# Kernel optimization log

Hardware: AMD Instinct MI355X
Metric: run time of the kernel (lower is better)

## Reference

```python
import jax, jax.numpy as jnp
import numpy as np

# ---- module hyperparameters (from init_kwargs) ----
K_CURV = 1.0      # Lorentz curvature k
MAX_NORM = 1000.0 # rescale_to_max cap on space-norm (assumed)
KSIZE = 5
STRIDE = 2
PAD = 2
IN_CH = 257       # includes time dim -> 256 space channels
OUT_CH = 257
LIN_FEATS = (IN_CH - 1) * KSIZE + 1  # 1281
EPS = 1e-8


def _add_time(space):
    # time = sqrt(k + ||space||^2), concat on last axis
    time = jnp.sqrt(K_CURV + jnp.sum(space * space, axis=-1, keepdims=True))
    return jnp.concatenate([time, space], axis=-1)


def _rescale_to_max(x):
    # clamp space-norm to MAX_NORM, then recompute valid time component
    space = x[..., 1:]
    norm = jnp.sqrt(jnp.sum(space * space, axis=-1, keepdims=True))
    scale = jnp.minimum(1.0, MAX_NORM / jnp.maximum(norm, EPS))
    return _add_time(space * scale)


def setup_inputs() -> dict:
    key = jax.random.key(0)
    kx, kw, kb = jax.random.split(key, 3)
    x = jax.random.normal(kx, (16, 8192, IN_CH), dtype=jnp.float32)
    W = jax.random.normal(kw, (OUT_CH, LIN_FEATS), dtype=jnp.float32) * 0.02
    b = jax.random.normal(kb, (OUT_CH,), dtype=jnp.float32) * 0.01
    return {"x": x, "W": W, "b": b}


def reference(x, W, b):
    B, L, C = x.shape
    # pad length dim with zeros (time channel of padded frames is clamped in
    # torch, but the time channel is discarded before add_time, so only the
    # space channels matter)
    xp = jnp.pad(x, ((0, 0), (PAD, PAD), (0, 0)))
    space = xp[..., 1:]                                  # (B, Lp, C-1)
    Lp = L + 2 * PAD
    n_frames = (Lp - KSIZE) // STRIDE + 1
    # im2col gather: (n_frames, K) window indices
    idx = jnp.arange(n_frames)[:, None] * STRIDE + jnp.arange(KSIZE)[None, :]
    patches = space[:, idx, :]                           # (B, n, K, C-1)
    # torch reorders to kernel-major (k, c) layout before add_time
    ps = patches.reshape(B, n_frames, KSIZE * (C - 1))   # (B, n, K*(C-1))
    pk = _add_time(ps)                                   # (B, n, lin_feats)
    out = jnp.einsum('bnf,of->bno', pk, W) + b           # LorentzProjection
    out = _add_time(out[..., 1:])                        # manifold.projx
    out = _rescale_to_max(out)                           # rescale_after=True
    return out
```

## Files before the change

### kernel.cpp

```cpp
#include <hip/hip_runtime.h>
#include <hip/hip_bf16.h>
#include <cstdint>
#include <cstddef>

namespace {

constexpr int BATCH = 16;
constexpr int LEN   = 8192;
constexpr int CIN   = 257;
constexpr int CS    = 256;
constexpr int NF    = 4096;
constexpr int LPAD  = LEN + 4;
constexpr int KG    = 1280;
constexpr int MT    = 64;

constexpr size_t XS_ELEMS  = (size_t)BATCH * LPAD * CS;
constexpr size_t XS_BYTES  = XS_ELEMS * 2;
constexpr size_t RSQ_OFF   = XS_BYTES;
constexpr size_t RSQ_BYTES = (size_t)BATCH * LPAD * 4;
constexpr size_t WT_OFF    = RSQ_OFF + RSQ_BYTES;
constexpr size_t WT_BYTES  = (size_t)CS * KG * 2;
constexpr size_t W0_OFF    = WT_OFF + WT_BYTES;
constexpr size_t WS_NEED   = W0_OFF + (size_t)CS * 4;

typedef __attribute__((ext_vector_type(8))) short short8;
typedef __attribute__((ext_vector_type(4))) float f32x4;

__device__ __forceinline__ unsigned short f2bf_bits(float f) {
  union { __hip_bfloat16 h; unsigned short u; } cv;
  cv.h = __float2bfloat16(f);
  return cv.u;
}

__device__ __forceinline__ void async_cp16(const void* g, void* l) {
  __builtin_amdgcn_global_load_lds(
      (const __attribute__((address_space(1))) void*)g,
      (__attribute__((address_space(3))) void*)l,
      16, 0, 0);
}

}

__global__ void prep_w_kernel(const float* __restrict__ W,
                              __hip_bfloat16* __restrict__ wt,
                              float* __restrict__ w0) {
  int n = blockIdx.x;
  const float* wrow = W + (size_t)(n + 1) * 1281;
  for (int k = threadIdx.x; k < KG; k += blockDim.x)
    wt[(size_t)n * KG + k] = __float2bfloat16(wrow[1 + k]);
  if (threadIdx.x == 0) w0[n] = wrow[0];
}

__global__ void prep_x_kernel(const float* __restrict__ x,
                              __hip_bfloat16* __restrict__ xs,
                              float* __restrict__ rowsq) {
  const int tid = threadIdx.x;
  const int bx  = blockIdx.x;
  if (bx < (BATCH * LEN) / 4) {
    int r    = bx * 4 + (tid >> 6);
    int lane = tid & 63;
    int b    = r >> 13;
    int t    = r & (LEN - 1);
    size_t tpg = (size_t)b * LPAD + 2 + t;
    const float* src = x + (size_t)r * CIN + 1 + lane * 4;
    float f0 = src[0], f1 = src[1], f2 = src[2], f3 = src[3];
    float s = f0 * f0 + f1 * f1 + f2 * f2 + f3 * f3;
    ushort4 pk;
    pk.x = f2bf_bits(f0); pk.y = f2bf_bits(f1);
    pk.z = f2bf_bits(f2); pk.w = f2bf_bits(f3);
    *(ushort4*)(xs + tpg * CS + lane * 4) = pk;
    for (int off = 32; off > 0; off >>= 1) s += __shfl_down(s, off);
    if (lane == 0) rowsq[tpg] = s;
  } else {
    for (int i = tid; i < 64 * 128; i += 256) {
      int row = i >> 7, u = i & 127;
      int b = row >> 2, j = row & 3;
      size_t tpg = (size_t)b * LPAD + (j < 2 ? j : 8192 + j);
      ((uint32_t*)xs)[tpg * 128 + u] = 0;
      if (u == 0) rowsq[tpg] = 0.0f;
    }
  }
}

__global__ __launch_bounds__(256, 3) void lorentz_gemm_kernel(
    const __hip_bfloat16* __restrict__ xs,
    const __hip_bfloat16* __restrict__ wt,
    const float* __restrict__ rowsq,
    const float* __restrict__ w0,
    const float* __restrict__ bvec,
    float* __restrict__ out) {
  __shared__ alignas(16) char lds[8192 + 32768];
  __shared__ alignas(16) float time0_s[64];
  __shared__ alignas(16) float normsq_s[64];
  char* A_lds = lds;
  char* B_lds = lds + 8192;

  const int tid   = threadIdx.x;
  const int w     = tid >> 6;
  const int lane  = tid & 63;
  const int row16 = lane & 15;
  const int q     = lane >> 4;

  const int bx    = blockIdx.x;
  const int b     = bx >> 6;
  const int Mbase = (bx & 63) * MT;

  const __hip_bfloat16* xsb = xs + ((size_t)b * LPAD + 2 * Mbase) * CS;

  f32x4 acc[4][4];
#pragma unroll
  for (int i = 0; i < 4; ++i)
#pragma unroll
    for (int j = 0; j < 4; ++j) acc[i][j] = (f32x4){0.f, 0.f, 0.f, 0.f};

  const int csw = (lane & 7) ^ (lane >> 3);

  for (int it = 0; it < 20; ++it) {
    const int kk = it >> 2;
    const int c0 = (it & 3) << 6;
    const int k0 = it << 6;
    __syncthreads();
#pragma unroll
    for (int j = 0; j < 2; ++j) {
      int m = w * 16 + j * 8 + (lane >> 3);
      const void* g = xsb + (size_t)(2 * m + kk) * CS + c0 + csw * 8;
      async_cp16(g, A_lds + (w * 2 + j) * 1024);
    }
#pragma unroll
    for (int j = 0; j < 8; ++j) {
      int n = w * 64 + j * 8 + (lane >> 3);
      const void* g = wt + (size_t)n * KG + k0 + csw * 8;
      async_cp16(g, B_lds + (w * 8 + j) * 1024);
    }
    __syncthreads();
#pragma unroll
    for (int s = 0; s < 2; ++s) {
      const int p = (s * 4 + q) ^ (lane & 7);
      short8 af[4], bf[4];
#pragma unroll
      for (int mt = 0; mt < 4; ++mt)
        af[mt] = *(const short8*)(A_lds + ((mt * 16 + row16) * 8 + p) * 16);
#pragma unroll
      for (int nt = 0; nt < 4; ++nt)
        bf[nt] = *(const short8*)(B_lds + ((w * 64 + nt * 16 + row16) * 8 + p) * 16);
#pragma unroll
      for (int mt = 0; mt < 4; ++mt)
#pragma unroll
        for (int nt = 0; nt < 4; ++nt)
          acc[mt][nt] = __builtin_amdgcn_mfma_f32_16x16x32_bf16(
              af[mt], bf[nt], acc[mt][nt], 0, 0, 0);
    }
  }

  if (tid < 64) {
    const float* rs = rowsq + (size_t)b * LPAD + 2 * (Mbase + tid);
    float s5 = rs[0] + rs[1] + rs[2] + rs[3] + rs[4];
    time0_s[tid] = sqrtf(1.0f + s5);
    normsq_s[tid] = 0.0f;
  }
  __syncthreads();

  float w0v[4], bv[4];
#pragma unroll
  for (int nt = 0; nt < 4; ++nt) {
    int n = w * 64 + nt * 16 + row16;
    w0v[nt] = w0[n];
    bv[nt]  = bvec[1 + n];
  }

#pragma unroll
  for (int mt = 0; mt < 4; ++mt) {
    f32x4 t4 = *(const f32x4*)&time0_s[mt * 16 + q * 4];
#pragma unroll
    for (int nt = 0; nt < 4; ++nt)
#pragma unroll
      for (int r = 0; r < 4; ++r)
        acc[mt][nt][r] = acc[mt][nt][r] + t4[r] * w0v[nt] + bv[nt];
#pragma unroll
    for (int r = 0; r < 4; ++r) {
      float ps = 0.f;
#pragma unroll
      for (int nt = 0; nt < 4; ++nt) ps += acc[mt][nt][r] * acc[mt][nt][r];
      ps += __shfl_xor(ps, 1);
      ps += __shfl_xor(ps, 2);
      ps += __shfl_xor(ps, 4);
      ps += __shfl_xor(ps, 8);
      if (row16 == 0) atomicAdd(&normsq_s[mt * 16 + q * 4 + r], ps);
    }
  }
  __syncthreads();

#pragma unroll
  for (int mt = 0; mt < 4; ++mt) {
#pragma unroll
    for (int r = 0; r < 4; ++r) {
      int m = mt * 16 + q * 4 + r;
      float nsq  = normsq_s[m];
      float norm = sqrtf(nsq);
      float scale = fminf(1.0f, 1000.0f / fmaxf(norm, 1e-8f));
      size_t ob = ((size_t)b * NF + Mbase + m) * 257;
#pragma unroll
      for (int nt = 0; nt < 4; ++nt) {
        int n = w * 64 + nt * 16 + row16;
        out[ob + 1 + n] = acc[mt][nt][r] * scale;
      }
    }
  }
  if (tid < 64) {
    float nsq  = normsq_s[tid];
    float norm = sqrtf(nsq);
    float scale = fminf(1.0f, 1000.0f / fmaxf(norm, 1e-8f));
    size_t ob = ((size_t)b * NF + Mbase + tid) * 257;
    out[ob] = sqrtf(1.0f + scale * scale * nsq);
  }
}

__global__ void fallback_kernel(const float* __restrict__ x,
                                const float* __restrict__ W,
                                const float* __restrict__ bvec,
                                float* __restrict__ out) {
  int fid = blockIdx.x;
  int b = fid >> 12;
  int g = fid & (NF - 1);
  __shared__ float patch[1280];
  __shared__ float red[256];
  int tid = threadIdx.x;
  float ss = 0.f;
  for (int k = tid; k < 1280; k += 256) {
    int kk = k >> 8, c = k & 255;
    int t = 2 * g + kk - 2;
    float v = (t >= 0 && t < LEN) ? x[((size_t)b * LEN + t) * CIN + 1 + c] : 0.f;
    patch[k] = v;
    ss += v * v;
  }
  red[tid] = ss;
  __syncthreads();
  for (int off = 128; off > 0; off >>= 1) {
    if (tid < off) red[tid] += red[tid + off];
    __syncthreads();
  }
  float time0 = sqrtf(1.f + red[0]);
  __syncthreads();
  const float* wrow = W + (size_t)(tid + 1) * 1281;
  float acc = time0 * wrow[0] + bvec[tid + 1];
  for (int k = 0; k < 1280; ++k) acc += wrow[1 + k] * patch[k];
  red[tid] = acc * acc;
  __syncthreads();
  for (int off = 128; off > 0; off >>= 1) {
    if (tid < off) red[tid] += red[tid + off];
    __syncthreads();
  }
  float nsq = red[0];
  float norm = sqrtf(nsq);
  float scale = fminf(1.f, 1000.f / fmaxf(norm, 1e-8f));
  size_t ob = ((size_t)b * NF + g) * 257;
  out[ob + 1 + tid] = acc * scale;
  if (tid == 0) out[ob] = sqrtf(1.f + scale * scale * nsq);
}

extern "C" void kernel_launch(void* const* d_in, const int* in_sizes, int n_in,
                              void* d_out, int out_size, void* d_ws, size_t ws_size,
                              hipStream_t stream) {
  const float* x  = (const float*)d_in[0];
  const float* W  = (const float*)d_in[1];
  const float* bv = (const float*)d_in[2];
  float* out = (float*)d_out;

  if (ws_size >= WS_NEED) {
    char* ws = (char*)d_ws;
    __hip_bfloat16* xs = (__hip_bfloat16*)ws;
    float* rowsq       = (float*)(ws + RSQ_OFF);
    __hip_bfloat16* wt = (__hip_bfloat16*)(ws + WT_OFF);
    float* w0          = (float*)(ws + W0_OFF);
    prep_w_kernel<<<256, 256, 0, stream>>>(W, wt, w0);
    prep_x_kernel<<<(BATCH * LEN) / 4 + 1, 256, 0, stream>>>(x, xs, rowsq);
    lorentz_gemm_kernel<<<BATCH * (NF / MT), 256, 0, stream>>>(xs, wt, rowsq, w0, bv, out);
  } else {
    fallback_kernel<<<BATCH * NF, 256, 0, stream>>>(x, W, bv, out);
  }
}
```

Before: 281.1 us.

## Double GEMM M-tile to 128 with 8 waves and stage prep_x rows through LDS

The GEMM kernel now covers 128 output frames per block with 512 threads arranged as 2×4 waves. Each W tile loaded into LDS is therefore reused across twice as many rows, which halves the per-frame W traffic and block count. Separately, prep_x now loads 16 full input rows per block into shared memory with coalesced float4 reads, then converts them to bf16 with 16-byte stores. This replaces the earlier misaligned scalar loads. The larger block uses more LDS and registers per block, and the launch-bounds change could reduce occupancy.

Measured after the change: 272.3 us. 1.03x faster.

```diff
diff --git a/kernel.cpp b/kernel.cpp
--- a/kernel.cpp
+++ b/kernel.cpp
@@ -12,7 +12,7 @@
 constexpr int NF    = 4096;
 constexpr int LPAD  = LEN + 4;
 constexpr int KG    = 1280;
-constexpr int MT    = 64;
+constexpr int MT    = 128;
 
 constexpr size_t XS_ELEMS  = (size_t)BATCH * LPAD * CS;
 constexpr size_t XS_BYTES  = XS_ELEMS * 2;
@@ -24,6 +24,7 @@
 constexpr size_t WS_NEED   = W0_OFF + (size_t)CS * 4;
 
 typedef __attribute__((ext_vector_type(8))) short short8;
+typedef __attribute__((ext_vector_type(8))) unsigned short ushort8v;
 typedef __attribute__((ext_vector_type(4))) float f32x4;
 
 __device__ __forceinline__ unsigned short f2bf_bits(float f) {
@@ -56,56 +57,78 @@
                               float* __restrict__ rowsq) {
   const int tid = threadIdx.x;
   const int bx  = blockIdx.x;
-  if (bx < (BATCH * LEN) / 4) {
-    int r    = bx * 4 + (tid >> 6);
-    int lane = tid & 63;
-    int b    = r >> 13;
-    int t    = r & (LEN - 1);
-    size_t tpg = (size_t)b * LPAD + 2 + t;
-    const float* src = x + (size_t)r * CIN + 1 + lane * 4;
-    float f0 = src[0], f1 = src[1], f2 = src[2], f3 = src[3];
-    float s = f0 * f0 + f1 * f1 + f2 * f2 + f3 * f3;
-    ushort4 pk;
-    pk.x = f2bf_bits(f0); pk.y = f2bf_bits(f1);
-    pk.z = f2bf_bits(f2); pk.w = f2bf_bits(f3);
-    *(ushort4*)(xs + tpg * CS + lane * 4) = pk;
-    for (int off = 32; off > 0; off >>= 1) s += __shfl_down(s, off);
-    if (lane == 0) rowsq[tpg] = s;
+  if (bx < 8192) {
+    __shared__ float4 xf4[1028];
+    const float4* src = (const float4*)(x + (size_t)bx * 4112);
+#pragma unroll
+    for (int i = 0; i < 4; ++i) {
+      int idx = i * 256 + tid;
+      xf4[idx] = src[idx];
+    }
+    if (tid < 4) xf4[1024 + tid] = src[1024 + tid];
+    __syncthreads();
+    const float* xf = (const float*)xf4;
+    const int row = tid >> 4, seg = tid & 15;
+    const float* v = xf + row * 257 + 1 + seg * 16;
+    float ss = 0.f;
+    unsigned short u[16];
+#pragma unroll
+    for (int i = 0; i < 16; ++i) {
+      float f = v[i];
+      ss += f * f;
+      u[i] = f2bf_bits(f);
+    }
+    const int b = bx >> 9;
+    const int t = (bx & 511) * 16 + row;
+    const size_t tpg = (size_t)b * LPAD + 2 + t;
+    ushort8v* dst = (ushort8v*)((unsigned short*)xs + tpg * CS + seg * 16);
+    ushort8v p0, p1;
+#pragma unroll
+    for (int i = 0; i < 8; ++i) { p0[i] = u[i]; p1[i] = u[8 + i]; }
+    dst[0] = p0;
+    dst[1] = p1;
+    ss += __shfl_xor(ss, 1);
+    ss += __shfl_xor(ss, 2);
+    ss += __shfl_xor(ss, 4);
+    ss += __shfl_xor(ss, 8);
+    if (seg == 0) rowsq[tpg] = ss;
   } else {
     for (int i = tid; i < 64 * 128; i += 256) {
-      int row = i >> 7, u = i & 127;
+      int row = i >> 7, uo = i & 127;
       int b = row >> 2, j = row & 3;
       size_t tpg = (size_t)b * LPAD + (j < 2 ? j : 8192 + j);
-      ((uint32_t*)xs)[tpg * 128 + u] = 0;
-      if (u == 0) rowsq[tpg] = 0.0f;
-    }
-  }
-}
-
-__global__ __launch_bounds__(256, 3) void lorentz_gemm_kernel(
+      ((uint32_t*)xs)[tpg * 128 + uo] = 0;
+      if (uo == 0) rowsq[tpg] = 0.0f;
+    }
+  }
+}
+
+__global__ __launch_bounds__(512, 4) void lorentz_gemm_kernel(
     const __hip_bfloat16* __restrict__ xs,
     const __hip_bfloat16* __restrict__ wt,
     const float* __restrict__ rowsq,
     const float* __restrict__ w0,
     const float* __restrict__ bvec,
     float* __restrict__ out) {
-  __shared__ alignas(16) char lds[8192 + 32768];
-  __shared__ alignas(16) float time0_s[64];
-  __shared__ alignas(16) float normsq_s[64];
+  __shared__ alignas(16) char lds[16384 + 32768];
+  __shared__ alignas(16) float time0_s[128];
+  __shared__ alignas(16) float normsq_s[128];
   char* A_lds = lds;
-  char* B_lds = lds + 8192;
+  char* B_lds = lds + 16384;
 
   const int tid   = threadIdx.x;
   const int w     = tid >> 6;
   const int lane  = tid & 63;
   const int row16 = lane & 15;
   const int q     = lane >> 4;
+  const int mh    = w >> 2;
+  const int nq    = w & 3;
 
   const int bx    = blockIdx.x;
-  const int b     = bx >> 6;
-  const int Mbase = (bx & 63) * MT;
-
-  const __hip_bfloat16* xsb = xs + ((size_t)b * LPAD + 2 * Mbase) * CS;
+  const int b     = bx >> 5;
+  const int Mblk  = (bx & 31) * MT;
+
+  const __hip_bfloat16* xsb = xs + ((size_t)b * LPAD + 2 * Mblk) * CS;
 
   f32x4 acc[4][4];
 #pragma unroll
@@ -127,33 +150,33 @@
       async_cp16(g, A_lds + (w * 2 + j) * 1024);
     }
 #pragma unroll
-    for (int j = 0; j < 8; ++j) {
-      int n = w * 64 + j * 8 + (lane >> 3);
+    for (int j = 0; j < 4; ++j) {
+      int n = w * 32 + j * 8 + (lane >> 3);
       const void* g = wt + (size_t)n * KG + k0 + csw * 8;
-      async_cp16(g, B_lds + (w * 8 + j) * 1024);
+      async_cp16(g, B_lds + (w * 4 + j) * 1024);
     }
     __syncthreads();
 #pragma unroll
     for (int s = 0; s < 2; ++s) {
       const int p = (s * 4 + q) ^ (lane & 7);
-      short8 af[4], bf[4];
-#pragma unroll
-      for (int mt = 0; mt < 4; ++mt)
-        af[mt] = *(const short8*)(A_lds + ((mt * 16 + row16) * 8 + p) * 16);
+      short8 bfr[4];
 #pragma unroll
       for (int nt = 0; nt < 4; ++nt)
-        bf[nt] = *(const short8*)(B_lds + ((w * 64 + nt * 16 + row16) * 8 + p) * 16);
-#pragma unroll
-      for (int mt = 0; mt < 4; ++mt)
+        bfr[nt] = *(const short8*)(B_lds + ((nq * 64 + nt * 16 + row16) * 8 + p) * 16);
+#pragma unroll
+      for (int mt = 0; mt < 4; ++mt) {
+        short8 af = *(const short8*)(A_lds + ((mh * 64 + mt * 16 + row16) * 8 + p) * 16);
 #pragma unroll
         for (int nt = 0; nt < 4; ++nt)
           acc[mt][nt] = __builtin_amdgcn_mfma_f32_16x16x32_bf16(
-              af[mt], bf[nt], acc[mt][nt], 0, 0, 0);
-    }
-  }
-
-  if (tid < 64) {
-    const float* rs = rowsq + (size_t)b * LPAD + 2 * (Mbase + tid);
+              af, bfr[nt], acc[mt][nt], 0, 0, 0);
+      }
+    }
+  }
+
+  __syncthreads();
+  if (tid < 128) {
+    const float* rs = rowsq + (size_t)b * LPAD + 2 * (Mblk + tid);
     float s5 = rs[0] + rs[1] + rs[2] + rs[3] + rs[4];
     time0_s[tid] = sqrtf(1.0f + s5);
     normsq_s[tid] = 0.0f;
@@ -163,14 +186,14 @@
   float w0v[4], bv[4];
 #pragma unroll
   for (int nt = 0; nt < 4; ++nt) {
-    int n = w * 64 + nt * 16 + row16;
+    int n = nq * 64 + nt * 16 + row16;
     w0v[nt] = w0[n];
     bv[nt]  = bvec[1 + n];
   }
 
 #pragma unroll
   for (int mt = 0; mt < 4; ++mt) {
-    f32x4 t4 = *(const f32x4*)&time0_s[mt * 16 + q * 4];
+    f32x4 t4 = *(const f32x4*)&time0_s[mh * 64 + mt * 16 + q * 4];
 #pragma unroll
     for (int nt = 0; nt < 4; ++nt)
 #pragma unroll
@@ -185,7 +208,7 @@
       ps += __shfl_xor(ps, 2);
       ps += __shfl_xor(ps, 4);
       ps += __shfl_xor(ps, 8);
-      if (row16 == 0) atomicAdd(&normsq_s[mt * 16 + q * 4 + r], ps);
+      if (row16 == 0) atomicAdd(&normsq_s[mh * 64 + mt * 16 + q * 4 + r], ps);
     }
   }
   __syncthreads();
@@ -194,23 +217,23 @@
   for (int mt = 0; mt < 4; ++mt) {
 #pragma unroll
     for (int r = 0; r < 4; ++r) {
-      int m = mt * 16 + q * 4 + r;
+      int m = mh * 64 + mt * 16 + q * 4 + r;
       float nsq  = normsq_s[m];
       float norm = sqrtf(nsq);
       float scale = fminf(1.0f, 1000.0f / fmaxf(norm, 1e-8f));
-      size_t ob = ((size_t)b * NF + Mbase + m) * 257;
+      size_t ob = ((size_t)b * NF + Mblk + m) * 257;
 #pragma unroll
       for (int nt = 0; nt < 4; ++nt) {
-        int n = w * 64 + nt * 16 + row16;
+        int n = nq * 64 + nt * 16 + row16;
         out[ob + 1 + n] = acc[mt][nt][r] * scale;
       }
     }
   }
-  if (tid < 64) {
+  if (tid < 128) {
     float nsq  = normsq_s[tid];
     float norm = sqrtf(nsq);
     float scale = fminf(1.0f, 1000.0f / fmaxf(norm, 1e-8f));
-    size_t ob = ((size_t)b * NF + Mbase + tid) * 257;
+    size_t ob = ((size_t)b * NF + Mblk + tid) * 257;
     out[ob] = sqrtf(1.0f + scale * scale * nsq);
   }
 }
@@ -273,8 +296,8 @@
     __hip_bfloat16* wt = (__hip_bfloat16*)(ws + WT_OFF);
     float* w0          = (float*)(ws + W0_OFF);
     prep_w_kernel<<<256, 256, 0, stream>>>(W, wt, w0);
-    prep_x_kernel<<<(BATCH * LEN) / 4 + 1, 256, 0, stream>>>(x, xs, rowsq);
-    lorentz_gemm_kernel<<<BATCH * (NF / MT), 256, 0, stream>>>(xs, wt, rowsq, w0, bv, out);
+    prep_x_kernel<<<8193, 256, 0, stream>>>(x, xs, rowsq);
+    lorentz_gemm_kernel<<<BATCH * (NF / MT), 512, 0, stream>>>(xs, wt, rowsq, w0, bv, out);
   } else {
     fallback_kernel<<<BATCH * NF, 256, 0, stream>>>(x, W, bv, out);
   }
```
